# Kernel tuning notes

Measured on AMD Instinct MI355X. Metric: run time of the kernel, lower is better.

## Reference

```python
import jax, jax.numpy as jnp
import numpy as np

N_NODES = 100000
N_EDGES = 3200000
F_IN, F_HID, N_CLASS = 512, 256, 41


def gcn_conv(x, edge_src, edge_dst, W, b, n_nodes):
    """PyG GCNConv: self-loops + symmetric deg^-1/2 normalization, then
    linear transform, gather-scale-scatter aggregation, bias add."""
    # add self loops
    loop = jnp.arange(n_nodes, dtype=edge_src.dtype)
    src = jnp.concatenate([edge_src, loop])
    dst = jnp.concatenate([edge_dst, loop])
    # degree (with self loops) on destination nodes
    deg = jax.ops.segment_sum(jnp.ones_like(dst, dtype=x.dtype), dst,
                              num_segments=n_nodes)
    dinv = deg ** -0.5  # deg >= 1 thanks to self loops
    norm = dinv[src] * dinv[dst]  # [E+N]
    h = x @ W  # [N, F_out]
    # gather-scale-scatter: out[dst] += norm * h[src]
    out = jax.ops.segment_sum(h[src] * norm[:, None], dst,
                              num_segments=n_nodes)
    return out + b


def setup_inputs() -> dict:
    key = jax.random.key(0)
    k1, k2, k3, k4 = jax.random.split(key, 4)
    x = jax.random.normal(k1, (N_NODES, F_IN), dtype=jnp.float32)
    edge_index = jax.random.randint(k2, (2, N_EDGES), 0, N_NODES, dtype=jnp.int64)
    W1 = jax.random.normal(k3, (F_IN, F_HID), dtype=jnp.float32) * (1.0 / np.sqrt(F_IN))
    b1 = jnp.zeros((F_HID,), dtype=jnp.float32)
    W2 = jax.random.normal(k4, (F_HID, N_CLASS), dtype=jnp.float32) * (1.0 / np.sqrt(F_HID))
    b2 = jnp.zeros((N_CLASS,), dtype=jnp.float32)
    return {"x": x, "edge_index": edge_index, "W1": W1, "b1": b1,
            "W2": W2, "b2": b2}


def reference(x, edge_index, W1, b1, W2, b2):
    src, dst = edge_index[0], edge_index[1]
    h = gcn_conv(x, src, dst, W1, b1, N_NODES)
    h = jax.nn.relu(h)
    # dropout omitted (eval mode / training=False)
    h = gcn_conv(h, src, dst, W2, b2, N_NODES)
    return jax.nn.log_softmax(h, axis=1)
```

## Files before the change

kernel.cpp:

```cpp
#include <hip/hip_runtime.h>
#include <math.h>

#define F_IN   512
#define F_HID  256
#define N_CLS  41

#define CHUNK  16384
#define MAXBK  3200
#define PKMASK 0x1FFFF
#define STILE_SH 12
#define NKEY   1024

typedef __attribute__((ext_vector_type(8))) short     bf16x8;
typedef __attribute__((ext_vector_type(8))) unsigned short u16x8;
typedef __attribute__((ext_vector_type(4))) float     f32x4;

__device__ __forceinline__ float b2f(unsigned short u) {
    union { unsigned int i; float f; } v; v.i = ((unsigned int)u) << 16; return v.f;
}
__device__ __forceinline__ unsigned short f2b(float f) {
    unsigned int u = __float_as_uint(f);
    u = (u + 0x7fffu + ((u >> 16) & 1u)) >> 16;
    return (unsigned short)u;
}

__global__ __launch_bounds__(256) void hist_pass(const int* __restrict__ edst,
                                                 int* __restrict__ hist_g,
                                                 int E, int NBK, int NW) {
    __shared__ int lh[MAXBK];
    int t = threadIdx.x, w = blockIdx.x;
    for (int b = t; b < NBK; b += 256) lh[b] = 0;
    __syncthreads();
    int e0 = w * CHUNK;
#pragma unroll 4
    for (int i = 0; i < CHUNK / 256; i++) {
        int e = e0 + i * 256 + t;
        if (e < E) atomicAdd(&lh[edst[e] >> 5], 1);
    }
    __syncthreads();
    for (int b = t; b < NBK; b += 256) hist_g[(size_t)b * NW + w] = lh[b];
}

__global__ __launch_bounds__(256) void s1_btot(const int* __restrict__ hist_g,
                                               int* __restrict__ btot,
                                               int NBK, int NW) {
    int b = blockIdx.x * 256 + threadIdx.x;
    if (b >= NBK) return;
    const int* row = &hist_g[(size_t)b * NW];
    int s = 0;
    for (int w = 0; w < NW; w++) s += row[w];
    btot[b] = s;
}

__global__ __launch_bounds__(256) void s2_scan(const int* __restrict__ btot,
                                               int* __restrict__ bbase, int NBK) {
    __shared__ int ls[MAXBK];
    __shared__ int ss[257];
    int t = threadIdx.x;
    const int CH = (MAXBK + 255) / 256;
    for (int b = t; b < NBK; b += 256) ls[b] = btot[b];
    __syncthreads();
    int s = 0;
    for (int i = 0; i < CH; i++) {
        int idx = t * CH + i;
        if (idx < NBK) s += ls[idx];
    }
    ss[t] = s;
    __syncthreads();
    if (t == 0) {
        int run = 0;
        for (int i = 0; i < 256; i++) { int v = ss[i]; ss[i] = run; run += v; }
        ss[256] = run;
    }
    __syncthreads();
    int run = ss[t];
    for (int i = 0; i < CH; i++) {
        int idx = t * CH + i;
        if (idx < NBK) { int v = ls[idx]; ls[idx] = run; run += v; }
    }
    __syncthreads();
    for (int b = t; b < NBK; b += 256) bbase[b] = ls[b];
    if (t == 0) bbase[NBK] = ss[256];
}

__global__ __launch_bounds__(256) void s3_rowscan(int* __restrict__ hist_g,
                                                  const int* __restrict__ bbase,
                                                  int NBK, int NW) {
    int b = blockIdx.x * 256 + threadIdx.x;
    if (b >= NBK) return;
    int* row = &hist_g[(size_t)b * NW];
    int run = bbase[b];
    for (int w = 0; w < NW; w++) { int v = row[w]; row[w] = run; run += v; }
}

__global__ __launch_bounds__(256) void scatter_pass(const int* __restrict__ esrc,
                                                    const int* __restrict__ edst,
                                                    const int* __restrict__ hist_g,
                                                    int* __restrict__ packed,
                                                    int E, int NBK, int NW) {
    __shared__ int cur[MAXBK];
    int t = threadIdx.x, w = blockIdx.x;
    for (int b = t; b < NBK; b += 256) cur[b] = hist_g[(size_t)b * NW + w];
    __syncthreads();
    int e0 = w * CHUNK;
#pragma unroll 4
    for (int i = 0; i < CHUNK / 256; i++) {
        int e = e0 + i * 256 + t;
        if (e < E) {
            int d = edst[e];
            int pos = atomicAdd(&cur[d >> 5], 1);
            packed[pos] = esrc[e] | ((d & 31) << 17);
        }
    }
}

__global__ __launch_bounds__(256) void bucket_sort(const int* __restrict__ packed,
                                                   const int* __restrict__ bbase,
                                                   int* __restrict__ packed2,
                                                   int* __restrict__ rp,
                                                   float* __restrict__ dinv, int M) {
    __shared__ int cnt[NKEY];
    __shared__ int ss[256];
    __shared__ int rtot[32];
    int b = blockIdx.x, t = threadIdx.x;
    int start = bbase[b], end = bbase[b + 1];
    for (int i = t; i < NKEY; i += 256) cnt[i] = 0;
    __syncthreads();
    for (int e = start + t; e < end; e += 256) {
        int p = packed[e];
        atomicAdd(&cnt[(((p >> 17) & 31) << 5) | ((p & PKMASK) >> STILE_SH)], 1);
    }
    __syncthreads();
    if (t < 32) {
        int s = 0;
#pragma unroll
        for (int i = 0; i < 32; i++) s += cnt[(t << 5) + i];
        rtot[t] = s;
        int node = (b << 5) + t;
        if (node < M) dinv[node] = rsqrtf((float)s + 1.0f);
    }
    int i0 = t << 2;
    int v0 = cnt[i0], v1 = cnt[i0 + 1], v2 = cnt[i0 + 2], v3 = cnt[i0 + 3];
    ss[t] = v0 + v1 + v2 + v3;
    __syncthreads();
    if (t == 0) {
        int run = start;
#pragma unroll
        for (int i = 0; i < 32; i++) {
            run += rtot[i];
            int node = (b << 5) + i;
            if (node < M) rp[node] = run;
        }
        run = start;
        for (int i = 0; i < 256; i++) { int v = ss[i]; ss[i] = run; run += v; }
    }
    __syncthreads();
    int run = ss[t];
    cnt[i0] = run; run += v0;
    cnt[i0 + 1] = run; run += v1;
    cnt[i0 + 2] = run; run += v2;
    cnt[i0 + 3] = run;
    __syncthreads();
    for (int e = start + t; e < end; e += 256) {
        int p = packed[e];
        int pos = atomicAdd(&cnt[(((p >> 17) & 31) << 5) | ((p & PKMASK) >> STILE_SH)], 1);
        packed2[pos] = p;
    }
}


__global__ __launch_bounds__(256) void cvt_W1t(const float* __restrict__ W1,
                                               unsigned short* __restrict__ W1t) {
    int n = blockIdx.x;
    for (int k = threadIdx.x; k < F_IN; k += 256)
        W1t[n * F_IN + k] = f2b(W1[(size_t)k * F_HID + n]);
}

__global__ __launch_bounds__(256) void cvt_W2t(const float* __restrict__ W2,
                                               unsigned short* __restrict__ W2t) {
    int n = blockIdx.x;
    int k = threadIdx.x;
    W2t[n * F_HID + k] = (n < N_CLS) ? f2b(W2[(size_t)k * N_CLS + n])
                                     : (unsigned short)0;
}


__global__ __launch_bounds__(512) void mfma_gemm1(const float* __restrict__ A,
                                                  const unsigned short* __restrict__ Bt,
                                                  const float* __restrict__ dinv,
                                                  unsigned short* __restrict__ H1,
                                                  int M) {
    __shared__ unsigned short As[128 * 40];
    __shared__ unsigned short Bs[256 * 40];
    int tid = threadIdx.x;
    int wave = tid >> 6, lane = tid & 63;
    int quad = lane >> 4, l15 = lane & 15;
    int m0 = blockIdx.x * 128;
    int wm = (wave & 1) * 64, wn = (wave >> 1) * 64;

    f32x4 acc[4][4] = {};

    int ar = tid >> 2, aq = tid & 3;
    int bn = tid >> 1, bc = tid & 1;

    for (int k0 = 0; k0 < F_IN; k0 += 32) {
        {
            int gm = m0 + ar;
            float4 v0, v1;
            if (gm < M) {
                const float4* ap = (const float4*)&A[(size_t)gm * F_IN + k0 + aq * 8];
                v0 = ap[0]; v1 = ap[1];
            } else {
                v0 = v1 = make_float4(0.f, 0.f, 0.f, 0.f);
            }
            u16x8 w;
            w[0]=f2b(v0.x); w[1]=f2b(v0.y); w[2]=f2b(v0.z); w[3]=f2b(v0.w);
            w[4]=f2b(v1.x); w[5]=f2b(v1.y); w[6]=f2b(v1.z); w[7]=f2b(v1.w);
            *(u16x8*)&As[ar * 40 + aq * 8] = w;
        }
        {
            const unsigned short* bp = &Bt[(size_t)bn * F_IN + k0];
            *(u16x8*)&Bs[bn * 40 + bc * 8]       = *(const u16x8*)(bp + bc * 8);
            *(u16x8*)&Bs[bn * 40 + (bc + 2) * 8] = *(const u16x8*)(bp + bc * 8 + 16);
        }
        __syncthreads();
        bf16x8 af[4], bfr[4];
#pragma unroll
        for (int i = 0; i < 4; i++)
            af[i] = *(const bf16x8*)&As[(wm + i * 16 + l15) * 40 + quad * 8];
#pragma unroll
        for (int j = 0; j < 4; j++)
            bfr[j] = *(const bf16x8*)&Bs[(wn + j * 16 + l15) * 40 + quad * 8];
#pragma unroll
        for (int i = 0; i < 4; i++)
#pragma unroll
            for (int j = 0; j < 4; j++)
                acc[i][j] = __builtin_amdgcn_mfma_f32_16x16x32_bf16(
                    af[i], bfr[j], acc[i][j], 0, 0, 0);
        __syncthreads();
    }
#pragma unroll
    for (int i = 0; i < 4; i++) {
#pragma unroll
        for (int rr = 0; rr < 4; rr++) {
            int gm = m0 + wm + i * 16 + quad * 4 + rr;
            if (gm < M) {
                float dv = dinv[gm];
#pragma unroll
                for (int j = 0; j < 4; j++) {
                    int gn = wn + j * 16 + l15;
                    H1[(size_t)gm * F_HID + gn] = f2b(dv * acc[i][j][rr]);
                }
            }
        }
    }
}


__global__ __launch_bounds__(256) void csr_agg1_fused(const int* __restrict__ rp,
                                                      const int* __restrict__ col,
                                                      const float* __restrict__ dinv,
                                                      const unsigned short* __restrict__ h1,
                                                      const float* __restrict__ b1,
                                                      const unsigned short* __restrict__ W2t,
                                                      unsigned short* __restrict__ h2b,
                                                      int M) {
    __shared__ unsigned short a4[4][256];
    int w = threadIdx.x >> 6, lane = threadIdx.x & 63;
    int r = blockIdx.x * 4 + w;
    bool valid = r < M;
    int start = 0, end = 0;
    float dr = 0.f;
    if (valid) {
        start = r ? rp[r - 1] : 0;
        end = rp[r];
        dr = dinv[r];
    }

    const ushort4* hv = (const ushort4*)h1;
    float ax = 0.f, ay = 0.f, az = 0.f, aw = 0.f;
    if (valid) {
        ushort4 v = hv[(size_t)r * 64 + lane];
        ax = b2f(v.x); ay = b2f(v.y); az = b2f(v.z); aw = b2f(v.w);
    }

    int e = start;
    for (; e + 8 <= end; e += 8) {
        int s0 = col[e]     & PKMASK, s1 = col[e + 1] & PKMASK;
        int s2 = col[e + 2] & PKMASK, s3 = col[e + 3] & PKMASK;
        int s4 = col[e + 4] & PKMASK, s5 = col[e + 5] & PKMASK;
        int s6 = col[e + 6] & PKMASK, s7 = col[e + 7] & PKMASK;
        ushort4 q0 = hv[(size_t)s0 * 64 + lane];
        ushort4 q1 = hv[(size_t)s1 * 64 + lane];
        ushort4 q2 = hv[(size_t)s2 * 64 + lane];
        ushort4 q3 = hv[(size_t)s3 * 64 + lane];
        ushort4 q4 = hv[(size_t)s4 * 64 + lane];
        ushort4 q5 = hv[(size_t)s5 * 64 + lane];
        ushort4 q6 = hv[(size_t)s6 * 64 + lane];
        ushort4 q7 = hv[(size_t)s7 * 64 + lane];
        ax += ((b2f(q0.x) + b2f(q1.x)) + (b2f(q2.x) + b2f(q3.x)))
            + ((b2f(q4.x) + b2f(q5.x)) + (b2f(q6.x) + b2f(q7.x)));
        ay += ((b2f(q0.y) + b2f(q1.y)) + (b2f(q2.y) + b2f(q3.y)))
            + ((b2f(q4.y) + b2f(q5.y)) + (b2f(q6.y) + b2f(q7.y)));
        az += ((b2f(q0.z) + b2f(q1.z)) + (b2f(q2.z) + b2f(q3.z)))
            + ((b2f(q4.z) + b2f(q5.z)) + (b2f(q6.z) + b2f(q7.z)));
        aw += ((b2f(q0.w) + b2f(q1.w)) + (b2f(q2.w) + b2f(q3.w)))
            + ((b2f(q4.w) + b2f(q5.w)) + (b2f(q6.w) + b2f(q7.w)));
    }
    for (; e < end; e++) {
        ushort4 q = hv[(size_t)(col[e] & PKMASK) * 64 + lane];
        ax += b2f(q.x); ay += b2f(q.y); az += b2f(q.z); aw += b2f(q.w);
    }
    if (valid) {
        float4 bb = *(const float4*)&b1[lane * 4];
        ushort4 o;
        o.x = f2b(fmaxf(dr * ax + bb.x, 0.f));
        o.y = f2b(fmaxf(dr * ay + bb.y, 0.f));
        o.z = f2b(fmaxf(dr * az + bb.z, 0.f));
        o.w = f2b(fmaxf(dr * aw + bb.w, 0.f));
        *(ushort4*)&a4[w][lane * 4] = o;
    }
    __syncthreads();
    if (w == 0) {
        int quad = lane >> 4, l15 = lane & 15;
        int rr4 = l15 & 3;
        f32x4 acc[3] = {};
#pragma unroll
        for (int kt = 0; kt < F_HID; kt += 32) {
            bf16x8 af = *(const bf16x8*)&a4[rr4][kt + quad * 8];
#pragma unroll
            for (int j = 0; j < 3; j++) {
                bf16x8 bf = *(const bf16x8*)&W2t[(size_t)(j * 16 + l15) * F_HID + kt + quad * 8];
                acc[j] = __builtin_amdgcn_mfma_f32_16x16x32_bf16(af, bf, acc[j], 0, 0, 0);
            }
        }
        if (quad == 0) {
#pragma unroll
            for (int rr = 0; rr < 4; rr++) {
                int gr = blockIdx.x * 4 + rr;
                if (gr < M) {
                    float dv = dinv[gr];
#pragma unroll
                    for (int j = 0; j < 3; j++) {
                        int c = j * 16 + l15;
                        h2b[(size_t)gr * 64 + c] = f2b(dv * acc[j][rr]);
                    }
                }
            }
        }
    }
}


__global__ __launch_bounds__(256) void csr_agg2_lsm(const int* __restrict__ rp,
                                                    const int* __restrict__ col,
                                                    const float* __restrict__ dinv,
                                                    const unsigned short* __restrict__ h2b,
                                                    const float* __restrict__ b2,
                                                    float* __restrict__ out, int M) {
    int w = threadIdx.x >> 6, lane = threadIdx.x & 63;
    int r = blockIdx.x * 4 + w;
    if (r >= M) return;
    int start = r ? rp[r - 1] : 0;
    int end = rp[r];
    float dr = dinv[r];
    int g = lane >> 4, l15 = lane & 15;
    bool act = l15 < 11;

    const ushort4* hq = (const ushort4*)h2b;
    float a0 = 0.f, a1 = 0.f, a2 = 0.f, a3 = 0.f;
    if (g == 0 && act) {
        ushort4 q = hq[(size_t)r * 16 + l15];
        a0 = b2f(q.x); a1 = b2f(q.y); a2 = b2f(q.z); a3 = b2f(q.w);
    }
    int e = start;
    for (; e + 8 <= end; e += 8) {
        int sA = col[e + g] & PKMASK;
        int sB = col[e + 4 + g] & PKMASK;
        if (act) {
            ushort4 qA = hq[(size_t)sA * 16 + l15];
            ushort4 qB = hq[(size_t)sB * 16 + l15];
            a0 += b2f(qA.x) + b2f(qB.x);
            a1 += b2f(qA.y) + b2f(qB.y);
            a2 += b2f(qA.z) + b2f(qB.z);
            a3 += b2f(qA.w) + b2f(qB.w);
        }
    }
    if (e + g < end && act) {
        ushort4 q = hq[(size_t)(col[e + g] & PKMASK) * 16 + l15];
        a0 += b2f(q.x); a1 += b2f(q.y); a2 += b2f(q.z); a3 += b2f(q.w);
    }
    if (e + 4 + g < end && act) {
        ushort4 q = hq[(size_t)(col[e + 4 + g] & PKMASK) * 16 + l15];
        a0 += b2f(q.x); a1 += b2f(q.y); a2 += b2f(q.z); a3 += b2f(q.w);
    }
    a0 += __shfl_xor(a0, 16); a0 += __shfl_xor(a0, 32);
    a1 += __shfl_xor(a1, 16); a1 += __shfl_xor(a1, 32);
    a2 += __shfl_xor(a2, 16); a2 += __shfl_xor(a2, 32);
    a3 += __shfl_xor(a3, 16); a3 += __shfl_xor(a3, 32);

    int c0 = l15 * 4;
    int cc = c0 < N_CLS ? c0 : N_CLS - 1;
    float4 bb = make_float4(b2[cc], b2[(c0 + 1 < N_CLS) ? c0 + 1 : N_CLS - 1],
                            b2[(c0 + 2 < N_CLS) ? c0 + 2 : N_CLS - 1],
                            b2[(c0 + 3 < N_CLS) ? c0 + 3 : N_CLS - 1]);
    float v0 = (c0     < N_CLS) ? dr * a0 + bb.x : -INFINITY;
    float v1 = (c0 + 1 < N_CLS) ? dr * a1 + bb.y : -INFINITY;
    float v2 = (c0 + 2 < N_CLS) ? dr * a2 + bb.z : -INFINITY;
    float v3 = (c0 + 3 < N_CLS) ? dr * a3 + bb.w : -INFINITY;

    float m = fmaxf(fmaxf(v0, v1), fmaxf(v2, v3));
#pragma unroll
    for (int off = 1; off < 16; off <<= 1) m = fmaxf(m, __shfl_xor(m, off));
    float s = expf(v0 - m) + expf(v1 - m) + expf(v2 - m) + expf(v3 - m);
#pragma unroll
    for (int off = 1; off < 16; off <<= 1) s += __shfl_xor(s, off);
    float ls = m + logf(s);

    if (g == 0) {
        float* orow = &out[(size_t)r * N_CLS];
        if (c0 < N_CLS)     __builtin_nontemporal_store(v0 - ls, &orow[c0]);
        if (c0 + 1 < N_CLS) __builtin_nontemporal_store(v1 - ls, &orow[c0 + 1]);
        if (c0 + 2 < N_CLS) __builtin_nontemporal_store(v2 - ls, &orow[c0 + 2]);
        if (c0 + 3 < N_CLS) __builtin_nontemporal_store(v3 - ls, &orow[c0 + 3]);
    }
}


extern "C" void kernel_launch(void* const* d_in, const int* in_sizes, int n_in,
                              void* d_out, int out_size, void* d_ws, size_t ws_size,
                              hipStream_t stream) {
    const float* x  = (const float*)d_in[0];
    const int*   ei = (const int*)d_in[1];
    const float* W1 = (const float*)d_in[2];
    const float* b1 = (const float*)d_in[3];
    const float* W2 = (const float*)d_in[4];
    const float* b2 = (const float*)d_in[5];
    float* out = (float*)d_out;

    const int M = in_sizes[0] / F_IN;
    const int E = in_sizes[1] / 2;
    const int* esrc = ei;
    const int* edst = ei + E;

    const int NBK = (M + 31) / 32;
    const int NW  = (E + CHUNK - 1) / CHUNK;

    char* ws = (char*)d_ws;
    float*          dinv    = (float*)(ws);
    int*            rp      = (int*)  (ws +    400128);
    int*            bbase   = (int*)  (ws +    800256);
    int*            btot    = (int*)  (ws +    812800);
    int*            hist_g  = (int*)  (ws +    825344);
    int*            packed  = (int*)  (ws +   3275392ull);
    int*            packed2 = (int*)  (ws +  16075392ull);
    unsigned short* W1t     = (unsigned short*)(ws + 28875392ull);
    unsigned short* W2t     = (unsigned short*)(ws + 29137536ull);
    unsigned short* h1      = (unsigned short*)(ws + 29162112ull);
    unsigned short* h2b     = (unsigned short*)(ws + 80362112ull);

    hist_pass<<<NW, 256, 0, stream>>>(edst, hist_g, E, NBK, NW);
    s1_btot<<<(NBK + 255) / 256, 256, 0, stream>>>(hist_g, btot, NBK, NW);
    s2_scan<<<1, 256, 0, stream>>>(btot, bbase, NBK);
    s3_rowscan<<<(NBK + 255) / 256, 256, 0, stream>>>(hist_g, bbase, NBK, NW);
    scatter_pass<<<NW, 256, 0, stream>>>(esrc, edst, hist_g, packed, E, NBK, NW);
    bucket_sort<<<NBK, 256, 0, stream>>>(packed, bbase, packed2, rp, dinv, M);

    cvt_W1t<<<F_HID, 256, 0, stream>>>(W1, W1t);
    cvt_W2t<<<48, 256, 0, stream>>>(W2, W2t);

    mfma_gemm1<<<(M + 127) / 128, 512, 0, stream>>>(x, W1t, dinv, h1, M);
    csr_agg1_fused<<<(M + 3) / 4, 256, 0, stream>>>(rp, packed2, dinv, h1, b1,
                                                    W2t, h2b, M);

    csr_agg2_lsm<<<(M + 3) / 4, 256, 0, stream>>>(rp, packed2, dinv, h2b, b2, out, M);
}
```

Measured before the change: 889.3 us.

## Transpose histogram layout, parallelize scans, tile W1 transpose through LDS

The per-block histogram is stored block-major (w*NBK+b), so writes in hist_pass and reads in scatter_pass are coalesced, and the column-sum and rowscan kernels read coalesced across threads. The serial single-thread prefix scans in s2_scan and bucket_sort become Hillis-Steele shared-memory scans plus a wave shuffle scan for row pointers. The W1 transpose/convert kernel now uses 64x64 LDS tiles with float4 loads and 16-byte stores. These target preprocessing overhead; the parallel scan adds many barriers in exchange.

```diff
diff --git a/kernel.cpp b/kernel.cpp
--- a/kernel.cpp
+++ b/kernel.cpp
@@ -23,6 +23,7 @@
     u = (u + 0x7fffu + ((u >> 16) & 1u)) >> 16;
     return (unsigned short)u;
 }
+
 
 __global__ __launch_bounds__(256) void hist_pass(const int* __restrict__ edst,
                                                  int* __restrict__ hist_g,
@@ -38,7 +39,7 @@
         if (e < E) atomicAdd(&lh[edst[e] >> 5], 1);
     }
     __syncthreads();
-    for (int b = t; b < NBK; b += 256) hist_g[(size_t)b * NW + w] = lh[b];
+    for (int b = t; b < NBK; b += 256) hist_g[(size_t)w * NBK + b] = lh[b];
 }
 
 __global__ __launch_bounds__(256) void s1_btot(const int* __restrict__ hist_g,
@@ -46,16 +47,15 @@
                                                int NBK, int NW) {
     int b = blockIdx.x * 256 + threadIdx.x;
     if (b >= NBK) return;
-    const int* row = &hist_g[(size_t)b * NW];
     int s = 0;
-    for (int w = 0; w < NW; w++) s += row[w];
+    for (int w = 0; w < NW; w++) s += hist_g[(size_t)w * NBK + b];
     btot[b] = s;
 }
 
 __global__ __launch_bounds__(256) void s2_scan(const int* __restrict__ btot,
                                                int* __restrict__ bbase, int NBK) {
     __shared__ int ls[MAXBK];
-    __shared__ int ss[257];
+    __shared__ int ss[256];
     int t = threadIdx.x;
     const int CH = (MAXBK + 255) / 256;
     for (int b = t; b < NBK; b += 256) ls[b] = btot[b];
@@ -65,22 +65,24 @@
         int idx = t * CH + i;
         if (idx < NBK) s += ls[idx];
     }
-    ss[t] = s;
-    __syncthreads();
-    if (t == 0) {
-        int run = 0;
-        for (int i = 0; i < 256; i++) { int v = ss[i]; ss[i] = run; run += v; }
-        ss[256] = run;
-    }
-    __syncthreads();
-    int run = ss[t];
+    int own = s;
+    ss[t] = own;
+    __syncthreads();
+#pragma unroll
+    for (int off = 1; off < 256; off <<= 1) {
+        int add = (t >= off) ? ss[t - off] : 0;
+        __syncthreads();
+        ss[t] += add;
+        __syncthreads();
+    }
+    int run = ss[t] - own;
     for (int i = 0; i < CH; i++) {
         int idx = t * CH + i;
         if (idx < NBK) { int v = ls[idx]; ls[idx] = run; run += v; }
     }
     __syncthreads();
     for (int b = t; b < NBK; b += 256) bbase[b] = ls[b];
-    if (t == 0) bbase[NBK] = ss[256];
+    if (t == 0) bbase[NBK] = ss[255];
 }
 
 __global__ __launch_bounds__(256) void s3_rowscan(int* __restrict__ hist_g,
@@ -88,9 +90,12 @@
                                                   int NBK, int NW) {
     int b = blockIdx.x * 256 + threadIdx.x;
     if (b >= NBK) return;
-    int* row = &hist_g[(size_t)b * NW];
     int run = bbase[b];
-    for (int w = 0; w < NW; w++) { int v = row[w]; row[w] = run; run += v; }
+    for (int w = 0; w < NW; w++) {
+        int v = hist_g[(size_t)w * NBK + b];
+        hist_g[(size_t)w * NBK + b] = run;
+        run += v;
+    }
 }
 
 __global__ __launch_bounds__(256) void scatter_pass(const int* __restrict__ esrc,
@@ -100,7 +105,7 @@
                                                     int E, int NBK, int NW) {
     __shared__ int cur[MAXBK];
     int t = threadIdx.x, w = blockIdx.x;
-    for (int b = t; b < NBK; b += 256) cur[b] = hist_g[(size_t)b * NW + w];
+    for (int b = t; b < NBK; b += 256) cur[b] = hist_g[(size_t)w * NBK + b];
     __syncthreads();
     int e0 = w * CHUNK;
 #pragma unroll 4
@@ -123,6 +128,7 @@
     __shared__ int ss[256];
     __shared__ int rtot[32];
     int b = blockIdx.x, t = threadIdx.x;
+    int lane = t & 63;
     int start = bbase[b], end = bbase[b + 1];
     for (int i = t; i < NKEY; i += 256) cnt[i] = 0;
     __syncthreads();
@@ -141,21 +147,29 @@
     }
     int i0 = t << 2;
     int v0 = cnt[i0], v1 = cnt[i0 + 1], v2 = cnt[i0 + 2], v3 = cnt[i0 + 3];
-    ss[t] = v0 + v1 + v2 + v3;
-    __syncthreads();
-    if (t == 0) {
-        int run = start;
-#pragma unroll
-        for (int i = 0; i < 32; i++) {
-            run += rtot[i];
-            int node = (b << 5) + i;
-            if (node < M) rp[node] = run;
-        }
-        run = start;
-        for (int i = 0; i < 256; i++) { int v = ss[i]; ss[i] = run; run += v; }
-    }
-    __syncthreads();
-    int run = ss[t];
+    int own = v0 + v1 + v2 + v3;
+    ss[t] = own;
+    __syncthreads();
+#pragma unroll
+    for (int off = 1; off < 256; off <<= 1) {
+        int add = (t >= off) ? ss[t - off] : 0;
+        __syncthreads();
+        ss[t] += add;
+        __syncthreads();
+    }
+    if (t < 64) {
+        int rv = (lane < 32) ? rtot[lane] : 0;
+#pragma unroll
+        for (int off = 1; off < 32; off <<= 1) {
+            int n = __shfl_up(rv, off);
+            if (lane >= off) rv += n;
+        }
+        if (lane < 32) {
+            int node = (b << 5) + lane;
+            if (node < M) rp[node] = start + rv;
+        }
+    }
+    int run = start + ss[t] - own;
     cnt[i0] = run; run += v0;
     cnt[i0 + 1] = run; run += v1;
     cnt[i0 + 2] = run; run += v2;
@@ -171,9 +185,28 @@
 
 __global__ __launch_bounds__(256) void cvt_W1t(const float* __restrict__ W1,
                                                unsigned short* __restrict__ W1t) {
-    int n = blockIdx.x;
-    for (int k = threadIdx.x; k < F_IN; k += 256)
-        W1t[n * F_IN + k] = f2b(W1[(size_t)k * F_HID + n]);
+    __shared__ unsigned short tl[64][72];
+    int kt = (blockIdx.x >> 2) << 6;
+    int nt = (blockIdx.x & 3) << 6;
+    int t = threadIdx.x;
+    int kr = t >> 2, nseg = (t & 3) << 4;
+    const float4* src = (const float4*)&W1[(size_t)(kt + kr) * F_HID + nt + nseg];
+    float4 f0 = src[0], f1 = src[1], f2 = src[2], f3 = src[3];
+    unsigned short* d = &tl[kr][nseg];
+    d[0]=f2b(f0.x); d[1]=f2b(f0.y); d[2]=f2b(f0.z); d[3]=f2b(f0.w);
+    d[4]=f2b(f1.x); d[5]=f2b(f1.y); d[6]=f2b(f1.z); d[7]=f2b(f1.w);
+    d[8]=f2b(f2.x); d[9]=f2b(f2.y); d[10]=f2b(f2.z); d[11]=f2b(f2.w);
+    d[12]=f2b(f3.x); d[13]=f2b(f3.y); d[14]=f2b(f3.z); d[15]=f2b(f3.w);
+    __syncthreads();
+    int nr = t >> 2, kseg = (t & 3) << 4;
+    u16x8 o0, o1;
+#pragma unroll
+    for (int j = 0; j < 8; j++) o0[j] = tl[kseg + j][nr];
+#pragma unroll
+    for (int j = 0; j < 8; j++) o1[j] = tl[kseg + 8 + j][nr];
+    unsigned short* dst = &W1t[(size_t)(nt + nr) * F_IN + kt + kseg];
+    *(u16x8*)dst = o0;
+    *(u16x8*)(dst + 8) = o1;
 }
 
 __global__ __launch_bounds__(256) void cvt_W2t(const float* __restrict__ W2,
@@ -400,8 +433,8 @@
     a3 += __shfl_xor(a3, 16); a3 += __shfl_xor(a3, 32);
 
     int c0 = l15 * 4;
-    int cc = c0 < N_CLS ? c0 : N_CLS - 1;
-    float4 bb = make_float4(b2[cc], b2[(c0 + 1 < N_CLS) ? c0 + 1 : N_CLS - 1],
+    float4 bb = make_float4(b2[c0 < N_CLS ? c0 : N_CLS - 1],
+                            b2[(c0 + 1 < N_CLS) ? c0 + 1 : N_CLS - 1],
                             b2[(c0 + 2 < N_CLS) ? c0 + 2 : N_CLS - 1],
                             b2[(c0 + 3 < N_CLS) ? c0 + 3 : N_CLS - 1]);
     float v0 = (c0     < N_CLS) ? dr * a0 + bb.x : -INFINITY;
@@ -466,7 +499,7 @@
     scatter_pass<<<NW, 256, 0, stream>>>(esrc, edst, hist_g, packed, E, NBK, NW);
     bucket_sort<<<NBK, 256, 0, stream>>>(packed, bbase, packed2, rp, dinv, M);
 
-    cvt_W1t<<<F_HID, 256, 0, stream>>>(W1, W1t);
+    cvt_W1t<<<32, 256, 0, stream>>>(W1, W1t);
     cvt_W2t<<<48, 256, 0, stream>>>(W2, W2t);
 
     mfma_gemm1<<<(M + 127) / 128, 512, 0, stream>>>(x, W1t, dinv, h1, M);
```

Result: faster. 852.1 us (-4.2%).
